# Performance work log

Hardware: AMD Instinct MI355X
Metric: run time of the kernel (lower is better)

The kernel has to match this reference:

```python
import jax, jax.numpy as jnp
import numpy as np

B, D_in, D_hid, D_out, D_future = 1024, 1024, 1024, 512, 32


def _lin_init(key, out_d, in_d, k_scale):
    k = 1.0 / np.sqrt(k_scale)
    k1, k2 = jax.random.split(key)
    W = jax.random.uniform(k1, (out_d, in_d), minval=-k, maxval=k, dtype=jnp.float32)
    b = jax.random.uniform(k2, (out_d,), minval=-k, maxval=k, dtype=jnp.float32)
    return W, b


def _lstm_cell(x, h, c, W_ih, W_hh, b_ih, b_hh):
    # PyTorch LSTMCell gate order: i, f, g, o
    gates = x @ W_ih.T + b_ih + h @ W_hh.T + b_hh
    i, f, g, o = jnp.split(gates, 4, axis=1)
    c2 = jax.nn.sigmoid(f) * c + jax.nn.sigmoid(i) * jnp.tanh(g)
    h2 = jax.nn.sigmoid(o) * jnp.tanh(c2)
    return h2, c2


def setup_inputs() -> dict:
    key = jax.random.key(0)
    ks = jax.random.split(key, 16)
    x = jax.random.normal(ks[0], (B, D_in), dtype=jnp.float32)
    hx = jax.random.normal(ks[1], (B, D_hid), dtype=jnp.float32)
    cx = jax.random.normal(ks[2], (B, D_hid), dtype=jnp.float32)
    # Decoder LSTMCell(D_out -> D_hid); torch init scale 1/sqrt(hidden)
    W_ih_dec, b_ih_dec = _lin_init(ks[3], 4 * D_hid, D_out, D_hid)
    W_hh_dec, b_hh_dec = _lin_init(ks[4], 4 * D_hid, D_hid, D_hid)
    W_r0, b_r0 = _lin_init(ks[5], D_hid, D_hid, D_hid)
    W_rp, b_rp = _lin_init(ks[6], D_out, D_hid, D_hid)
    W_rr, b_rr = _lin_init(ks[7], D_out, D_out, D_out)
    W_s0, b_s0 = _lin_init(ks[8], D_in, D_hid, D_hid)
    # StaRNNCell LSTMCell(2*D_in -> D_hid)
    W_ih_sta, b_ih_sta = _lin_init(ks[9], 4 * D_hid, 2 * D_in, D_hid)
    W_hh_sta, b_hh_sta = _lin_init(ks[10], 4 * D_hid, D_hid, D_hid)
    W_sn, b_sn = _lin_init(ks[11], D_out, D_hid, D_hid)
    return dict(x=x, hx=hx, cx=cx,
                W_ih_dec=W_ih_dec, W_hh_dec=W_hh_dec, b_ih_dec=b_ih_dec, b_hh_dec=b_hh_dec,
                W_r0=W_r0, b_r0=b_r0, W_rp=W_rp, b_rp=b_rp, W_rr=W_rr, b_rr=b_rr,
                W_s0=W_s0, b_s0=b_s0,
                W_ih_sta=W_ih_sta, W_hh_sta=W_hh_sta, b_ih_sta=b_ih_sta, b_hh_sta=b_hh_sta,
                W_sn=W_sn, b_sn=b_sn)


def reference(x, hx, cx,
              W_ih_dec, W_hh_dec, b_ih_dec, b_hh_dec,
              W_r0, b_r0, W_rp, b_rp, W_rr, b_rr,
              W_s0, b_s0,
              W_ih_sta, W_hh_sta, b_ih_sta, b_hh_sta,
              W_sn, b_sn):
    ohx, ocx = hx, cx
    r0 = jnp.zeros((x.shape[0], D_out), dtype=x.dtype)
    hd0 = hx @ W_r0.T + b_r0  # LinLayerR0

    def step(carry, _):
        r, hd, cd = carry
        hd, cd = _lstm_cell(r, hd, cd, W_ih_dec, W_hh_dec, b_ih_dec, b_hh_dec)
        p = hd @ W_rp.T + b_rp    # LinLayerRp
        r = p @ W_rr.T + b_rr     # LinLayerRr
        return (r, hd, cd), (hd, p)

    _, (fts_bar, Act_bar) = jax.lax.scan(step, (r0, hd0, cx), None, length=D_future)
    # fts_bar: [D_future, B, D_hid]; AvgPool1d over D_future == mean over axis 0
    hbar = fts_bar.mean(axis=0)
    xbar = jax.nn.relu(hbar @ W_s0.T + b_s0)  # LinLayerS0 + relu
    xcat = jnp.concatenate([x, xbar], axis=1)
    hx2, cx2 = _lstm_cell(xcat, ohx, ocx, W_ih_sta, W_hh_sta, b_ih_sta, b_hh_sta)
    Act = hx2 @ W_sn.T + b_sn  # LinLayerSn
    return (Act, Act_bar, (hx2, cx2))
```

## Files before the change

### kernel.cpp

```cpp
#include <hip/hip_runtime.h>
#include <hip/hip_bf16.h>
#include <stdint.h>


typedef unsigned short ushort_t;
typedef __attribute__((ext_vector_type(8))) short short8;
typedef __attribute__((ext_vector_type(4))) float floatx4;

__device__ __forceinline__ unsigned short f2bf(float f) {
    unsigned int u = __float_as_uint(f);
    u += 0x7FFF + ((u >> 16) & 1);
    return (unsigned short)(u >> 16);
}
__device__ __forceinline__ float bf2f(unsigned short u) {
    return __uint_as_float(((unsigned int)u) << 16);
}
__device__ __forceinline__ float sigm(float x) { return 1.f / (1.f + __expf(-x)); }

__device__ __forceinline__ void glds16(const ushort_t* g, const ushort_t* l) {
    __builtin_amdgcn_global_load_lds(
        (const __attribute__((address_space(1))) uint32_t*)g,
        (__attribute__((address_space(3))) uint32_t*)l, 16, 0, 0);
}

__device__ __forceinline__ unsigned ld_rlx(const unsigned* p) {
    return __hip_atomic_load(p, __ATOMIC_RELAXED, __HIP_MEMORY_SCOPE_AGENT);
}

template <bool WF, bool WB, bool RELU, bool NT>
__global__ __launch_bounds__(256)
void gemm_bt(const ushort_t* __restrict__ A, int lda,
             const ushort_t* __restrict__ Bw, int ldb,
             int Kloop, int kzOff,
             const float* __restrict__ bias,
             float* __restrict__ Cf, int ldcf, size_t czStride,
             ushort_t* __restrict__ Cb, int ldcb) {
    __shared__ __align__(16) ushort_t As[128 * 32];
    __shared__ __align__(16) ushort_t Bs[128 * 32];
    const int t = threadIdx.x;
    const int l = t & 63;
    const int w = t >> 6;
    int bx = blockIdx.x, by = blockIdx.y;
    if ((gridDim.y & 7) == 0) {
        const int flat = bx + gridDim.x * by;
        const int xcd = flat & 7;
        const int j = flat >> 3;
        const int jm = j / gridDim.x;
        by = xcd * (gridDim.y >> 3) + jm;
        bx = j - jm * gridDim.x;
    }
    const int m0 = by << 7;
    const int n0 = bx << 7;
    const int kz = blockIdx.z;
    A  += (size_t)kz * kzOff;
    Bw += (size_t)kz * kzOff;
    if (WF) Cf += (size_t)kz * czStride;
    const int wm = (w >> 1) << 6;
    const int wn = (w & 1) << 6;
    const int lr = l & 15;
    const int lg = l >> 4;

    floatx4 acc[4][4] = {};

    const int srow = (w << 4) + (l >> 2);
    const int cc = ((l & 3) - ((l >> 3) & 3)) & 3;
    const int scol = cc << 3;
    const ushort_t* Ag0 = A + (size_t)(m0 + srow) * lda + scol;
    const ushort_t* Ag1 = A + (size_t)(m0 + 64 + srow) * lda + scol;
    const ushort_t* Bg0 = Bw + (size_t)(n0 + srow) * ldb + scol;
    const ushort_t* Bg1 = Bw + (size_t)(n0 + 64 + srow) * ldb + scol;
    const ushort_t* lA0 = &As[t * 8];
    const ushort_t* lA1 = &As[2048 + t * 8];
    const ushort_t* lB0 = &Bs[t * 8];
    const ushort_t* lB1 = &Bs[2048 + t * 8];

    int aoff[4], boff[4];
#pragma unroll
    for (int i = 0; i < 4; i++) {
        const int Ra = wm + i * 16 + lr;
        aoff[i] = ((Ra << 2) + ((lg + ((Ra >> 1) & 3)) & 3)) << 3;
        const int Rb = wn + i * 16 + lr;
        boff[i] = ((Rb << 2) + ((lg + ((Rb >> 1) & 3)) & 3)) << 3;
    }

    for (int kk = 0; kk < Kloop; kk += 32) {
        glds16(Ag0 + kk, lA0);
        glds16(Ag1 + kk, lA1);
        glds16(Bg0 + kk, lB0);
        glds16(Bg1 + kk, lB1);
        __syncthreads();
        short8 af[4], bfr[4];
#pragma unroll
        for (int i = 0; i < 4; i++) af[i] = *(const short8*)&As[aoff[i]];
#pragma unroll
        for (int j = 0; j < 4; j++) bfr[j] = *(const short8*)&Bs[boff[j]];
#pragma unroll
        for (int i = 0; i < 4; i++)
#pragma unroll
            for (int j = 0; j < 4; j++)
                acc[i][j] = __builtin_amdgcn_mfma_f32_16x16x32_bf16(af[i], bfr[j], acc[i][j], 0, 0, 0);
        __syncthreads();
    }

#pragma unroll
    for (int i = 0; i < 4; i++) {
#pragma unroll
        for (int j = 0; j < 4; j++) {
            const int col = n0 + wn + j * 16 + lr;
            const float bv = bias ? bias[col] : 0.f;
#pragma unroll
            for (int r = 0; r < 4; r++) {
                const int row = m0 + wm + i * 16 + lg * 4 + r;
                float v = acc[i][j][r] + bv;
                if (RELU) v = fmaxf(v, 0.f);
                if (WF) {
                    if (NT) __builtin_nontemporal_store(v, &Cf[(size_t)row * ldcf + col]);
                    else Cf[(size_t)row * ldcf + col] = v;
                }
                if (WB) Cb[(size_t)row * ldcb + col] = f2bf(v);
            }
        }
    }
}

template <bool HF, bool NT>
__global__ __launch_bounds__(256, 2)
void gates_fused(const ushort_t* __restrict__ A, int lda,
                 const ushort_t* __restrict__ WI, int K,
                 const float* __restrict__ biasI,
                 const float* __restrict__ cin, float* __restrict__ cout,
                 ushort_t* __restrict__ hbf, int ldh,
                 float* __restrict__ hf) {
    __shared__ __align__(16) float Cs[64 * 132];
    ushort_t* AsBase = (ushort_t*)Cs;
    const int t = threadIdx.x;
    const int l = t & 63;
    const int w = t >> 6;
    const int flat = blockIdx.x + (blockIdx.y << 5);
    const int xcd = flat & 7;
    const int jsw = flat >> 3;
    const int bn = (xcd << 2) + (jsw >> 4);
    const int bm = jsw & 15;
    const int m0 = bm << 6;
    const int n0 = bn << 7;
    const int u0 = bn << 5;
    const int lr = l & 15;
    const int lg = l >> 4;

    floatx4 acc[4][2] = {};

    const int srow = t >> 2;
    const int cc = ((t & 3) - ((t >> 3) & 3)) & 3;
    const int scol = cc << 3;
    const ushort_t* Ag = A + (size_t)(m0 + srow) * lda + scol;

    int aoff[4];
#pragma unroll
    for (int i = 0; i < 4; i++) {
        const int Ra = i * 16 + lr;
        aoff[i] = ((Ra << 2) + ((lg + ((Ra >> 1) & 3)) & 3)) << 3;
    }
    const ushort_t* BgW[2];
#pragma unroll
    for (int jf = 0; jf < 2; jf++)
        BgW[jf] = WI + (size_t)(n0 + (w << 5) + jf * 16 + lr) * K + (lg << 3);

    auto issueA = [&](int b, int sp) {
#pragma unroll
        for (int s = 0; s < 4; s++)
            glds16(Ag + sp * 128 + s * 32, AsBase + b * 8192 + s * 2048 + t * 8);
    };
    auto loadB = [&](short8 (&br)[4][2], int sp) {
#pragma unroll
        for (int s = 0; s < 4; s++)
#pragma unroll
            for (int jf = 0; jf < 2; jf++)
                br[s][jf] = *(const short8*)(BgW[jf] + sp * 128 + s * 32);
    };
    auto compute = [&](int b, short8 (&br)[4][2]) {
#pragma unroll
        for (int s = 0; s < 4; s++) {
            short8 af[4];
#pragma unroll
            for (int i = 0; i < 4; i++)
                af[i] = *(const short8*)(AsBase + b * 8192 + s * 2048 + aoff[i]);
#pragma unroll
            for (int i = 0; i < 4; i++)
#pragma unroll
                for (int jf = 0; jf < 2; jf++)
                    acc[i][jf] = __builtin_amdgcn_mfma_f32_16x16x32_bf16(af[i], br[s][jf], acc[i][jf], 0, 0, 0);
        }
    };

    short8 b0[4][2], b1[4][2];
    const int NS = K >> 7;
    issueA(0, 0);
    loadB(b0, 0);
    for (int sp = 0; sp < NS; sp += 2) {
        __syncthreads();
        if (sp + 1 < NS) { issueA(1, sp + 1); loadB(b1, sp + 1); }
        compute(0, b0);
        __syncthreads();
        if (sp + 2 < NS) { issueA(0, sp + 2); loadB(b0, sp + 2); }
        compute(1, b1);
    }
    __syncthreads();

#pragma unroll
    for (int i = 0; i < 4; i++)
#pragma unroll
        for (int jf = 0; jf < 2; jf++) {
            const int colb = (w << 5) + jf * 16 + lr;
#pragma unroll
            for (int r = 0; r < 4; r++)
                Cs[(i * 16 + lg * 4 + r) * 132 + colb] = acc[i][jf][r];
        }
    __syncthreads();

#pragma unroll
    for (int p = 0; p < 8; p++) {
        const int row = p * 8 + (t >> 5);
        const int uu = t & 31;
        const float4 g4 = *(const float4*)&Cs[row * 132 + uu * 4];
        const int grow = m0 + row;
        const int gu = u0 + uu;
        const float4 b4 = *(const float4*)&biasI[gu * 4];
        const float iv = sigm(g4.x + b4.x);
        const float fv = sigm(g4.y + b4.y);
        const float gv = tanhf(g4.z + b4.z);
        const float ov = sigm(g4.w + b4.w);
        const size_t cidx = (size_t)grow * 1024 + gu;
        const float c = fv * cin[cidx] + iv * gv;
        const float h = ov * tanhf(c);
        if (NT) __builtin_nontemporal_store(c, &cout[cidx]);
        else cout[cidx] = c;
        hbf[(size_t)grow * ldh + gu] = f2bf(h);
        if (HF) {
            if (NT) __builtin_nontemporal_store(h, &hf[cidx]);
            else hf[cidx] = h;
        }
    }
}

__global__ __launch_bounds__(256, 2)
void gates_persist(ushort_t* __restrict__ HD,
                   const ushort_t* __restrict__ Wh,
                   const ushort_t* __restrict__ Wg,
                   const float* __restrict__ biasD,
                   const float* __restrict__ biasG,
                   const float* __restrict__ cx,
                   ushort_t* __restrict__ hbarb,
                   unsigned* __restrict__ flags,
                   unsigned* __restrict__ gen) {
    const size_t SLOT = 1048576;
    __shared__ __align__(16) float Cs[64 * 132];
    ushort_t* AsBase = (ushort_t*)Cs;
    const int t = threadIdx.x;
    const int l = t & 63;
    const int w = t >> 6;
    const int bid = blockIdx.x;
    const int xcd = bid & 7;
    const int jsw = bid >> 3;
    const int bn = (xcd << 2) + (jsw >> 4);
    const int bm = jsw & 15;
    const int m0 = bm << 6;
    const int n0 = bn << 7;
    const int u0 = bn << 5;
    const int lr = l & 15;
    const int lg = l >> 4;

    const int srow = t >> 2;
    const int cc = ((t & 3) - ((t >> 3) & 3)) & 3;
    const int scol = cc << 3;
    const ushort_t* Ag = HD + (size_t)(m0 + srow) * 1024 + scol;

    int aoff[4];
#pragma unroll
    for (int i = 0; i < 4; i++) {
        const int Ra = i * 16 + lr;
        aoff[i] = ((Ra << 2) + ((lg + ((Ra >> 1) & 3)) & 3)) << 3;
    }

    const int uu = t & 31;
    const int gu = u0 + uu;
    const int rb = t >> 5;
    const float4 b4d = *(const float4*)&biasD[gu * 4];
    const float4 b4g = *(const float4*)&biasG[gu * 4];
    float cst[8], hsum[8];
#pragma unroll
    for (int p = 0; p < 8; p++) {
        cst[p] = cx[(size_t)(m0 + p * 8 + rb) * 1024 + gu];
        hsum[p] = 0.f;
    }

    for (int s = 0; s < 32; ++s) {
        if (s) {
            __syncthreads();
            if (t == 0)
                __hip_atomic_store(&flags[bid << 4], (unsigned)s,
                                   __ATOMIC_RELEASE, __HIP_MEMORY_SCOPE_AGENT);
            if (bid == 0) {
                while (ld_rlx(&flags[t << 4]) < (unsigned)s)
                    __builtin_amdgcn_s_sleep(2);
                while (ld_rlx(&flags[(t + 256) << 4]) < (unsigned)s)
                    __builtin_amdgcn_s_sleep(2);
                __syncthreads();
                if (t == 0)
                    __hip_atomic_store(gen, (unsigned)s,
                                       __ATOMIC_RELEASE, __HIP_MEMORY_SCOPE_AGENT);
            }
            if (t == 0) {
                while (ld_rlx(gen) < (unsigned)s)
                    __builtin_amdgcn_s_sleep(2);
            }
            __syncthreads();
        }

        const ushort_t* W = s ? Wg : Wh;
        const ushort_t* BgW[2];
#pragma unroll
        for (int jf = 0; jf < 2; jf++)
            BgW[jf] = W + (size_t)(n0 + (w << 5) + jf * 16 + lr) * 1024 + (lg << 3);

        floatx4 acc[4][2] = {};

        auto issueA = [&](int b, int sp) {
#pragma unroll
            for (int ss = 0; ss < 4; ss++)
                glds16(Ag + sp * 128 + ss * 32, AsBase + b * 8192 + ss * 2048 + t * 8);
        };
        auto loadB = [&](short8 (&br)[4][2], int sp) {
#pragma unroll
            for (int ss = 0; ss < 4; ss++)
#pragma unroll
                for (int jf = 0; jf < 2; jf++)
                    br[ss][jf] = *(const short8*)(BgW[jf] + sp * 128 + ss * 32);
        };
        auto compute = [&](int b, short8 (&br)[4][2]) {
#pragma unroll
            for (int ss = 0; ss < 4; ss++) {
                short8 af[4];
#pragma unroll
                for (int i = 0; i < 4; i++)
                    af[i] = *(const short8*)(AsBase + b * 8192 + ss * 2048 + aoff[i]);
#pragma unroll
                for (int i = 0; i < 4; i++)
#pragma unroll
                    for (int jf = 0; jf < 2; jf++)
                        acc[i][jf] = __builtin_amdgcn_mfma_f32_16x16x32_bf16(af[i], br[ss][jf], acc[i][jf], 0, 0, 0);
            }
        };

        short8 b0[4][2], b1[4][2];
        issueA(0, 0);
        loadB(b0, 0);
        for (int sp = 0; sp < 8; sp += 2) {
            __syncthreads();
            if (sp + 1 < 8) { issueA(1, sp + 1); loadB(b1, sp + 1); }
            compute(0, b0);
            __syncthreads();
            if (sp + 2 < 8) { issueA(0, sp + 2); loadB(b0, sp + 2); }
            compute(1, b1);
        }
        __syncthreads();

#pragma unroll
        for (int i = 0; i < 4; i++)
#pragma unroll
            for (int jf = 0; jf < 2; jf++) {
                const int colb = (w << 5) + jf * 16 + lr;
#pragma unroll
                for (int r = 0; r < 4; r++)
                    Cs[(i * 16 + lg * 4 + r) * 132 + colb] = acc[i][jf][r];
            }
        __syncthreads();

        ushort_t* Hout = HD + (size_t)(s + 1) * SLOT;
        const float4 b4 = s ? b4g : b4d;
#pragma unroll
        for (int p = 0; p < 8; p++) {
            const int row = p * 8 + rb;
            const float4 g4 = *(const float4*)&Cs[row * 132 + uu * 4];
            const float iv = sigm(g4.x + b4.x);
            const float fv = sigm(g4.y + b4.y);
            const float gv = tanhf(g4.z + b4.z);
            const float ov = sigm(g4.w + b4.w);
            cst[p] = fv * cst[p] + iv * gv;
            const float h = ov * tanhf(cst[p]);
            Hout[(size_t)(m0 + row) * 1024 + gu] = f2bf(h);
            hsum[p] += h;
        }
        Ag += SLOT;
    }

#pragma unroll
    for (int p = 0; p < 8; p++)
        hbarb[(size_t)(m0 + p * 8 + rb) * 1024 + gu] = f2bf(hsum[p] * (1.f / 32.f));
}

__global__ void zero_bar(unsigned* __restrict__ b, int n) {
    int i = blockIdx.x * 256 + threadIdx.x;
    if (i < n) b[i] = 0u;
}

__global__ void pack2_bf(ushort_t* __restrict__ dst, const float* __restrict__ s1, int K1,
                         const float* __restrict__ s2, int K2) {
    const int n = blockIdx.y;
    const int k = blockIdx.x * 256 + threadIdx.x;
    const int Kt = K1 + K2;
    float v = (k < K1) ? s1[(size_t)n * K1 + k] : s2[(size_t)n * K2 + (k - K1)];
    dst[(size_t)n * Kt + k] = f2bf(v);
}

__global__ void tpose_bf(ushort_t* __restrict__ dst, const float* __restrict__ src,
                         int R, int C) {
    const int c = blockIdx.y;
    const int r = blockIdx.x * 256 + threadIdx.x;
    dst[(size_t)c * R + r] = f2bf(src[(size_t)r * C + c]);
}

__global__ void ileave_whh_k(ushort_t* __restrict__ dst, const float* __restrict__ Whh) {
    const int rI = blockIdx.y;
    const int k = blockIdx.x * 256 + threadIdx.x;
    const int r = ((rI & 3) << 10) + (rI >> 2);
    dst[(size_t)rI * 1024 + k] = f2bf(Whh[(size_t)r * 1024 + k]);
}

__global__ void ileave_add_k(ushort_t* __restrict__ dst, const float* __restrict__ Wgf,
                             const float* __restrict__ Whh) {
    const int rI = blockIdx.y;
    const int k = blockIdx.x * 256 + threadIdx.x;
    const int r = ((rI & 3) << 10) + (rI >> 2);
    dst[(size_t)rI * 1024 + k] = f2bf(Wgf[(size_t)r * 1024 + k] + Whh[(size_t)r * 1024 + k]);
}

__global__ void ileave_sta_k(ushort_t* __restrict__ dst, const float* __restrict__ Wih,
                             const float* __restrict__ Whh) {
    const int rI = blockIdx.y;
    const int k = blockIdx.x * 256 + threadIdx.x;
    const int r = ((rI & 3) << 10) + (rI >> 2);
    float v = (k < 2048) ? Wih[(size_t)r * 2048 + k] : Whh[(size_t)r * 1024 + (k - 2048)];
    dst[(size_t)rI * 3072 + k] = f2bf(v);
}

__global__ void bias_il_k(float* __restrict__ dst, const float* __restrict__ b_ih,
                          const float* __restrict__ b_hh) {
    const int rI = blockIdx.x * 256 + threadIdx.x;
    const int r = ((rI & 3) << 10) + (rI >> 2);
    dst[rI] = b_ih[r] + b_hh[r];
}

__global__ void br2_k(float* __restrict__ br2, const float* __restrict__ Wrr,
                      const float* __restrict__ b_rp, const float* __restrict__ b_rr) {
    const int o = blockIdx.x * 256 + threadIdx.x;
    float s = b_rr[o];
    for (int m = 0; m < 512; m++) s += Wrr[o * 512 + m] * b_rp[m];
    br2[o] = s;
}

__global__ void biasg_k(float* __restrict__ dst, const float* __restrict__ Wih,
                        const float* __restrict__ b_ih, const float* __restrict__ b_hh,
                        const float* __restrict__ br2) {
    const int rI = blockIdx.x * 256 + threadIdx.x;
    const int r = ((rI & 3) << 10) + (rI >> 2);
    float s = b_ih[r] + b_hh[r];
    for (int o = 0; o < 512; o++) s += Wih[(size_t)r * 512 + o] * br2[o];
    dst[rI] = s;
}

__global__ void init_sta(const float* __restrict__ x, const float* __restrict__ hx,
                         ushort_t* __restrict__ A2) {
    int idx = blockIdx.x * 256 + threadIdx.x;
    int b = idx >> 10, j = idx & 1023;
    A2[(size_t)b * 3072 + j] = f2bf(x[idx]);
    A2[(size_t)b * 3072 + 2048 + j] = f2bf(hx[idx]);
}

extern "C" void kernel_launch(void* const* d_in, const int* in_sizes, int n_in,
                              void* d_out, int out_size, void* d_ws, size_t ws_size,
                              hipStream_t stream) {
    const float* x        = (const float*)d_in[0];
    const float* hx       = (const float*)d_in[1];
    const float* cx       = (const float*)d_in[2];
    const float* W_ih_dec = (const float*)d_in[3];
    const float* W_hh_dec = (const float*)d_in[4];
    const float* b_ih_dec = (const float*)d_in[5];
    const float* b_hh_dec = (const float*)d_in[6];
    const float* W_r0     = (const float*)d_in[7];
    const float* b_r0     = (const float*)d_in[8];
    const float* W_rp     = (const float*)d_in[9];
    const float* b_rp     = (const float*)d_in[10];
    const float* W_rr     = (const float*)d_in[11];
    const float* b_rr     = (const float*)d_in[12];
    const float* W_s0     = (const float*)d_in[13];
    const float* b_s0     = (const float*)d_in[14];
    const float* W_ih_sta = (const float*)d_in[15];
    const float* W_hh_sta = (const float*)d_in[16];
    const float* b_ih_sta = (const float*)d_in[17];
    const float* b_hh_sta = (const float*)d_in[18];
    const float* W_sn     = (const float*)d_in[19];
    const float* b_sn     = (const float*)d_in[20];
    float* out = (float*)d_out;

    float* Act    = out;
    float* ActBar = out + 524288;
    float* Hx2    = out + 524288 + 16777216;
    float* Cx2    = Hx2 + 1048576;

    char* ws = (char*)d_ws;
    size_t off = 0;
    auto alloc = [&](size_t bytes) -> void* {
        void* p = ws + off;
        off += (bytes + 255) & ~(size_t)255;
        return p;
    };
    const size_t SLOT = 1048576;
    ushort_t* HDall  = (ushort_t*)alloc(33ull * SLOT * 2);
    ushort_t* WgI    = (ushort_t*)alloc(4096ull * 1024 * 2);
    ushort_t* WhhI   = (ushort_t*)alloc(4096ull * 1024 * 2);
    ushort_t* WcatSI = (ushort_t*)alloc(4096ull * 3072 * 2);
    ushort_t* Wrpb   = (ushort_t*)alloc(512ull * 1024 * 2);
    ushort_t* Wr0b   = (ushort_t*)alloc(1024ull * 1024 * 2);
    ushort_t* Ws0b   = (ushort_t*)alloc(1024ull * 1024 * 2);
    ushort_t* Wsnb   = (ushort_t*)alloc(512ull * 1024 * 2);
    float*    biasDI = (float*)alloc(4096 * 4);
    float*    biasGI = (float*)alloc(4096 * 4);
    float*    biasSI = (float*)alloc(4096 * 4);
    float*    br2    = (float*)alloc(512 * 4);
    ushort_t* Acat2  = (ushort_t*)alloc(1024ull * 3072 * 2);
    ushort_t* hbarb  = (ushort_t*)alloc(1024ull * 1024 * 2);
    ushort_t* hx2b   = (ushort_t*)alloc(1024ull * 1024 * 2);
    unsigned* barws  = (unsigned*)alloc((512 * 16 + 16) * 4);
    if (ws_size < off) return;

    float*    Wgf    = (float*)(HDall + 1 * SLOT);
    ushort_t* Wihb   = HDall + 9 * SLOT;
    ushort_t* WrpT   = HDall + 11 * SLOT;
    ushort_t* Wrp2Tb = HDall + 11 * SLOT + 524288;
    ushort_t* Wrrb   = HDall + 12 * SLOT;

    zero_bar<<<33, 256, 0, stream>>>(barws, 512 * 16 + 16);
    init_sta<<<4096, 256, 0, stream>>>(x, hx, Acat2);
    pack2_bf<<<dim3(2, 512), 256, 0, stream>>>(Wrrb, W_rr, 512, nullptr, 0);
    pack2_bf<<<dim3(2, 4096), 256, 0, stream>>>(Wihb, W_ih_dec, 512, nullptr, 0);
    pack2_bf<<<dim3(4, 512), 256, 0, stream>>>(Wrpb, W_rp, 1024, nullptr, 0);
    pack2_bf<<<dim3(4, 1024), 256, 0, stream>>>(Wr0b, W_r0, 1024, nullptr, 0);
    pack2_bf<<<dim3(4, 1024), 256, 0, stream>>>(Ws0b, W_s0, 1024, nullptr, 0);
    pack2_bf<<<dim3(4, 512), 256, 0, stream>>>(Wsnb, W_sn, 1024, nullptr, 0);
    tpose_bf<<<dim3(2, 1024), 256, 0, stream>>>(WrpT, W_rp, 512, 1024);
    ileave_whh_k<<<dim3(4, 4096), 256, 0, stream>>>(WhhI, W_hh_dec);
    bias_il_k<<<16, 256, 0, stream>>>(biasDI, b_ih_dec, b_hh_dec);
    ileave_sta_k<<<dim3(12, 4096), 256, 0, stream>>>(WcatSI, W_ih_sta, W_hh_sta);
    bias_il_k<<<16, 256, 0, stream>>>(biasSI, b_ih_sta, b_hh_sta);
    br2_k<<<2, 256, 0, stream>>>(br2, W_rr, b_rp, b_rr);
    biasg_k<<<16, 256, 0, stream>>>(biasGI, W_ih_dec, b_ih_dec, b_hh_dec, br2);

    gemm_bt<false, true, false, false><<<dim3(4, 8, 1), 256, 0, stream>>>(
        WrpT, 512, Wrrb, 512, 512, 0, nullptr, nullptr, 0, 0, Wrp2Tb, 512);
    gemm_bt<true, false, false, false><<<dim3(8, 32, 1), 256, 0, stream>>>(
        Wihb, 512, Wrp2Tb, 512, 512, 0, nullptr, Wgf, 1024, 0, nullptr, 0);
    ileave_add_k<<<dim3(4, 4096), 256, 0, stream>>>(WgI, Wgf, W_hh_dec);

    gemm_bt<false, true, false, false><<<dim3(8, 8, 1), 256, 0, stream>>>(
        Acat2 + 2048, 3072, Wr0b, 1024, 1024, 0, b_r0, nullptr, 0, 0, HDall, 1024);

    gates_persist<<<512, 256, 0, stream>>>(
        HDall, WhhI, WgI, biasDI, biasGI, cx, hbarb, barws, barws + 512 * 16);

    gemm_bt<true, false, false, true><<<dim3(4, 256, 1), 256, 0, stream>>>(
        HDall + SLOT, 1024, Wrpb, 1024, 1024, 0, b_rp, ActBar, 512, 0, nullptr, 0);

    gemm_bt<false, true, true, false><<<dim3(8, 8, 1), 256, 0, stream>>>(
        hbarb, 1024, Ws0b, 1024, 1024, 0, b_s0, nullptr, 0, 0, Acat2 + 1024, 3072);

    gates_fused<true, true><<<dim3(32, 16), 256, 0, stream>>>(
        Acat2, 3072, WcatSI, 3072, biasSI, cx, Cx2, hx2b, 1024, Hx2);

    gemm_bt<true, false, false, true><<<dim3(4, 8, 1), 256, 0, stream>>>(
        hx2b, 1024, Wsnb, 1024, 1024, 0, b_sn, Act, 512, 0, nullptr, 0);

    (void)in_sizes; (void)n_in; (void)out_size;
}
```

Baseline: 1.381 ms.

## Replace global grid barrier with per-row-group flags in persistent LSTM kernel

```diff
diff --git a/kernel.cpp b/kernel.cpp
--- a/kernel.cpp
+++ b/kernel.cpp
@@ -242,37 +242,35 @@
     }
 }
 
-__global__ __launch_bounds__(256, 2)
-void gates_persist(ushort_t* __restrict__ HD,
-                   const ushort_t* __restrict__ Wh,
-                   const ushort_t* __restrict__ Wg,
-                   const float* __restrict__ biasD,
-                   const float* __restrict__ biasG,
-                   const float* __restrict__ cx,
-                   ushort_t* __restrict__ hbarb,
-                   unsigned* __restrict__ flags,
-                   unsigned* __restrict__ gen) {
+__global__ __launch_bounds__(512, 1)
+void gates_rows(ushort_t* __restrict__ HD,
+                const ushort_t* __restrict__ Wh,
+                const ushort_t* __restrict__ Wg,
+                const float* __restrict__ biasD,
+                const float* __restrict__ biasG,
+                const float* __restrict__ cx,
+                ushort_t* __restrict__ hbarb,
+                unsigned* __restrict__ flags) {
     const size_t SLOT = 1048576;
-    __shared__ __align__(16) float Cs[64 * 132];
+    __shared__ __align__(16) float Cs[64 * 260];
     ushort_t* AsBase = (ushort_t*)Cs;
     const int t = threadIdx.x;
     const int l = t & 63;
     const int w = t >> 6;
     const int bid = blockIdx.x;
-    const int xcd = bid & 7;
-    const int jsw = bid >> 3;
-    const int bn = (xcd << 2) + (jsw >> 4);
-    const int bm = jsw & 15;
-    const int m0 = bm << 6;
-    const int n0 = bn << 7;
-    const int u0 = bn << 5;
+    const int g = bid >> 4;
+    const int q = bid & 15;
+    const int m0 = g << 6;
+    const int n0 = q << 8;
+    const int u0 = q << 6;
     const int lr = l & 15;
     const int lg = l >> 4;
 
-    const int srow = t >> 2;
-    const int cc = ((t & 3) - ((t >> 3) & 3)) & 3;
-    const int scol = cc << 3;
-    const ushort_t* Ag = HD + (size_t)(m0 + srow) * 1024 + scol;
+    const int u8 = t & 255;
+    const int pr = t >> 8;
+    const int srow = u8 >> 2;
+    const int cc = ((u8 & 3) - ((u8 >> 3) & 3)) & 3;
+    const ushort_t* Ag = HD + (size_t)(m0 + srow) * 1024 + (cc << 3);
 
     int aoff[4];
 #pragma unroll
@@ -281,9 +279,9 @@
         aoff[i] = ((Ra << 2) + ((lg + ((Ra >> 1) & 3)) & 3)) << 3;
     }
 
-    const int uu = t & 31;
+    const int uu = t & 63;
     const int gu = u0 + uu;
-    const int rb = t >> 5;
+    const int rb = t >> 6;
     const float4 b4d = *(const float4*)&biasD[gu * 4];
     const float4 b4g = *(const float4*)&biasG[gu * 4];
     float cst[8], hsum[8];
@@ -295,24 +293,9 @@
 
     for (int s = 0; s < 32; ++s) {
         if (s) {
-            __syncthreads();
-            if (t == 0)
-                __hip_atomic_store(&flags[bid << 4], (unsigned)s,
-                                   __ATOMIC_RELEASE, __HIP_MEMORY_SCOPE_AGENT);
-            if (bid == 0) {
-                while (ld_rlx(&flags[t << 4]) < (unsigned)s)
+            if (t < 16)
+                while (ld_rlx(&flags[((g << 4) | t) << 4]) < (unsigned)s)
                     __builtin_amdgcn_s_sleep(2);
-                while (ld_rlx(&flags[(t + 256) << 4]) < (unsigned)s)
-                    __builtin_amdgcn_s_sleep(2);
-                __syncthreads();
-                if (t == 0)
-                    __hip_atomic_store(gen, (unsigned)s,
-                                       __ATOMIC_RELEASE, __HIP_MEMORY_SCOPE_AGENT);
-            }
-            if (t == 0) {
-                while (ld_rlx(gen) < (unsigned)s)
-                    __builtin_amdgcn_s_sleep(2);
-            }
             __syncthreads();
         }
 
@@ -326,8 +309,11 @@
 
         auto issueA = [&](int b, int sp) {
 #pragma unroll
-            for (int ss = 0; ss < 4; ss++)
-                glds16(Ag + sp * 128 + ss * 32, AsBase + b * 8192 + ss * 2048 + t * 8);
+            for (int j = 0; j < 2; j++) {
+                const int ss = pr * 2 + j;
+                glds16(Ag + sp * 128 + ss * 32,
+                       AsBase + b * 8192 + ss * 2048 + u8 * 8);
+            }
         };
         auto loadB = [&](short8 (&br)[4][2], int sp) {
 #pragma unroll
@@ -371,7 +357,7 @@
                 const int colb = (w << 5) + jf * 16 + lr;
 #pragma unroll
                 for (int r = 0; r < 4; r++)
-                    Cs[(i * 16 + lg * 4 + r) * 132 + colb] = acc[i][jf][r];
+                    Cs[(i * 16 + lg * 4 + r) * 260 + colb] = acc[i][jf][r];
             }
         __syncthreads();
 
@@ -380,7 +366,7 @@
 #pragma unroll
         for (int p = 0; p < 8; p++) {
             const int row = p * 8 + rb;
-            const float4 g4 = *(const float4*)&Cs[row * 132 + uu * 4];
+            const float4 g4 = *(const float4*)&Cs[row * 260 + uu * 4];
             const float iv = sigm(g4.x + b4.x);
             const float fv = sigm(g4.y + b4.y);
             const float gv = tanhf(g4.z + b4.z);
@@ -389,6 +375,13 @@
             const float h = ov * tanhf(cst[p]);
             Hout[(size_t)(m0 + row) * 1024 + gu] = f2bf(h);
             hsum[p] += h;
+        }
+
+        if (s < 31) {
+            __syncthreads();
+            if (t == 0)
+                __hip_atomic_store(&flags[((g << 4) | q) << 4], (unsigned)(s + 1),
+                                   __ATOMIC_RELEASE, __HIP_MEMORY_SCOPE_AGENT);
         }
         Ag += SLOT;
     }
@@ -530,7 +523,7 @@
     ushort_t* Acat2  = (ushort_t*)alloc(1024ull * 3072 * 2);
     ushort_t* hbarb  = (ushort_t*)alloc(1024ull * 1024 * 2);
     ushort_t* hx2b   = (ushort_t*)alloc(1024ull * 1024 * 2);
-    unsigned* barws  = (unsigned*)alloc((512 * 16 + 16) * 4);
+    unsigned* barws  = (unsigned*)alloc(256 * 16 * 4);
     if (ws_size < off) return;
 
     float*    Wgf    = (float*)(HDall + 1 * SLOT);
@@ -539,7 +532,7 @@
     ushort_t* Wrp2Tb = HDall + 11 * SLOT + 524288;
     ushort_t* Wrrb   = HDall + 12 * SLOT;
 
-    zero_bar<<<33, 256, 0, stream>>>(barws, 512 * 16 + 16);
+    zero_bar<<<16, 256, 0, stream>>>(barws, 256 * 16);
     init_sta<<<4096, 256, 0, stream>>>(x, hx, Acat2);
     pack2_bf<<<dim3(2, 512), 256, 0, stream>>>(Wrrb, W_rr, 512, nullptr, 0);
     pack2_bf<<<dim3(2, 4096), 256, 0, stream>>>(Wihb, W_ih_dec, 512, nullptr, 0);
@@ -564,8 +557,8 @@
     gemm_bt<false, true, false, false><<<dim3(8, 8, 1), 256, 0, stream>>>(
         Acat2 + 2048, 3072, Wr0b, 1024, 1024, 0, b_r0, nullptr, 0, 0, HDall, 1024);
 
-    gates_persist<<<512, 256, 0, stream>>>(
-        HDall, WhhI, WgI, biasDI, biasGI, cx, hbarb, barws, barws + 512 * 16);
+    gates_rows<<<256, 512, 0, stream>>>(
+        HDall, WhhI, WgI, biasDI, biasGI, cx, hbarb, barws);
 
     gemm_bt<true, false, false, true><<<dim3(4, 256, 1), 256, 0, stream>>>(
         HDall + SLOT, 1024, Wrpb, 1024, 1024, 0, b_rp, ActBar, 512, 0, nullptr, 0);
```

Result: faster. 1.327 ms (-3.9%).
